# Kernel optimization log

Measured on AMD Instinct MI355X. Metric: run time of the kernel, lower is better.

Reference implementation:

```python
import jax, jax.numpy as jnp
import numpy as np
from functools import partial

BETA_F = 1.0        # layer default beta_f
DOUBLING_ITERS = 21 # covers tree depth up to 2**21; random recursive tree depth ~ O(log N)


def setup_inputs() -> dict:
    key = jax.random.key(0)
    ks = jax.random.split(key, 6)
    N, K = 2_000_000, 8
    H, W = 2048, 2048
    attrs2d = jax.random.uniform(ks[0], (N, K), dtype=jnp.float32)  # normalized attrs in [a,1]
    weight = jax.random.normal(ks[1], (K,), dtype=jnp.float32)
    bias = jax.random.normal(ks[2], (1,), dtype=jnp.float32)
    levels = jax.random.uniform(ks[3], (N,), dtype=jnp.float32)
    # valid component tree: parent[i] < i for i>0, root = 0
    u = jax.random.uniform(ks[4], (N,))
    parent = jnp.floor(u * jnp.arange(N, dtype=jnp.float32)).astype(jnp.int32)
    pixel_node = jax.random.randint(ks[5], (H, W), 0, N, dtype=jnp.int32)
    return {"attrs2d": attrs2d, "weight": weight, "bias": bias,
            "levels": levels, "parent": parent, "pixel_node": pixel_node}


def _tree_filter(sigmoid, levels, parent, pixel_node):
    """Connected (direct-rule) filtering on a component tree.

    Each node contributes sigma(node) * (level(node) - level(parent));
    the filtered value of a pixel is the sum of contributions along the
    root-to-node path (root contributes its full level).
    Path sums are computed with pointer doubling (fully vectorized).
    """
    N = levels.shape[0]
    contrib = sigmoid * (levels - levels[parent])          # (N,)
    contrib = contrib.at[0].set(levels[0])                 # root keeps its level
    # sentinel node N with zero contribution, parent of root -> sentinel
    contrib_e = jnp.concatenate([contrib, jnp.zeros((1,), contrib.dtype)])
    par_e = jnp.concatenate([parent.at[0].set(N), jnp.array([N], jnp.int32)])

    def step(carry, _):
        s, p = carry
        return (s + s[p], p[p]), None

    (s, _), _ = jax.lax.scan(step, (contrib_e, par_e), None, length=DOUBLING_ITERS)
    y_nodes = s[:N]                                        # filtered gray value per node
    return y_nodes[pixel_node]                             # (H, W)


def reference(attrs2d, weight, bias, levels, parent, pixel_node):
    logits = attrs2d @ weight + bias[0]                    # (N,)
    s = BETA_F * logits                                    # clamp_logits=False (layer default)
    sigmoid = jax.nn.sigmoid(s)
    return _tree_filter(sigmoid, levels, parent, pixel_node)
```

## Files before the change

kernel.cpp:

```cpp
#include <hip/hip_runtime.h>
#include <hip/hip_fp16.h>

typedef float vf4 __attribute__((ext_vector_type(4)));
typedef int   vi4 __attribute__((ext_vector_type(4)));

struct SP { float s; int p; };

__device__ __forceinline__ SP ldSP(const SP* __restrict__ ptr) {
    float2 v = *reinterpret_cast<const float2*>(ptr);
    SP r; r.s = v.x; r.p = __float_as_int(v.y);
    return r;
}
__device__ __forceinline__ void stSP(SP* __restrict__ ptr, float s, int p) {
    float2 v; v.x = s; v.y = __int_as_float(p);
    *reinterpret_cast<float2*>(ptr) = v;
}

__global__ void k_lev16(const float* __restrict__ levels,
                        __half* __restrict__ lev, int N) {
    int stride = gridDim.x * blockDim.x;
    int n4 = N >> 2;
    const vf4* l4 = reinterpret_cast<const vf4*>(levels);
    __half2* h2 = reinterpret_cast<__half2*>(lev);
    for (int i = blockIdx.x * blockDim.x + threadIdx.x; i < n4; i += stride) {
        vf4 v = __builtin_nontemporal_load(&l4[i]);
        __half2 h0; h0.x = __float2half(v.x); h0.y = __float2half(v.y);
        __half2 h1; h1.x = __float2half(v.z); h1.y = __float2half(v.w);
        h2[2 * i]     = h0;
        h2[2 * i + 1] = h1;
    }
    for (int i = (n4 << 2) + blockIdx.x * blockDim.x + threadIdx.x; i < N; i += stride)
        lev[i] = __float2half(levels[i]);
}

__global__ void k_contrib(const float* __restrict__ attrs,
                          const float* __restrict__ weight,
                          const float* __restrict__ bias,
                          const float* __restrict__ levels,
                          const __half* __restrict__ lev,
                          const int*   __restrict__ parent,
                          SP* __restrict__ buf, int N) {
    float w0 = weight[0], w1 = weight[1], w2 = weight[2], w3 = weight[3];
    float w4 = weight[4], w5 = weight[5], w6 = weight[6], w7 = weight[7];
    float b = bias[0];
    int stride = gridDim.x * blockDim.x;
    const vf4* a4 = reinterpret_cast<const vf4*>(attrs);
    for (int i = blockIdx.x * blockDim.x + threadIdx.x; i < N; i += stride) {
        vf4 a0 = __builtin_nontemporal_load(&a4[2 * (size_t)i]);
        vf4 a1 = __builtin_nontemporal_load(&a4[2 * (size_t)i + 1]);
        float x = a0.x * w0 + a0.y * w1 + a0.z * w2 + a0.w * w3
                + a1.x * w4 + a1.y * w5 + a1.z * w6 + a1.w * w7 + b;
        float sg = 1.0f / (1.0f + __expf(-x));
        int p = __builtin_nontemporal_load(&parent[i]);
        float c = sg * (__half2float(lev[i]) - __half2float(lev[p]));
        if (i == 0) stSP(&buf[0], levels[0], N);
        else        stSP(&buf[i], c, p);
    }
}

__global__ void k_level(const SP* __restrict__ buf,
                        __half* __restrict__ y16,
                        int lo, int hi, int N) {
    int i = lo + blockIdx.x * blockDim.x + threadIdx.x;
    if (i >= hi) return;
    float acc = 0.0f;
    int p = i;
    while (p >= lo && p < N) {
        SP w = ldSP(&buf[p]);
        acc += w.s;
        p = w.p;
    }
    if (p < lo) acc += __half2float(y16[p]);
    y16[i] = __float2half(acc);
}

__global__ void k_gather(const __half* __restrict__ y,
                         const int*   __restrict__ pix,
                         float*       __restrict__ out, int M) {
    int stride = gridDim.x * blockDim.x;
    int M8 = M >> 3;
    const vi4* pix4 = reinterpret_cast<const vi4*>(pix);
    vf4* out4 = reinterpret_cast<vf4*>(out);
    for (int g = blockIdx.x * blockDim.x + threadIdx.x; g < M8; g += stride) {
        vi4 p0 = __builtin_nontemporal_load(&pix4[2 * g]);
        vi4 p1 = __builtin_nontemporal_load(&pix4[2 * g + 1]);
        vf4 o0, o1;
        o0.x = __half2float(y[p0.x]);
        o0.y = __half2float(y[p0.y]);
        o0.z = __half2float(y[p0.z]);
        o0.w = __half2float(y[p0.w]);
        o1.x = __half2float(y[p1.x]);
        o1.y = __half2float(y[p1.y]);
        o1.z = __half2float(y[p1.z]);
        o1.w = __half2float(y[p1.w]);
        __builtin_nontemporal_store(o0, &out4[2 * g]);
        __builtin_nontemporal_store(o1, &out4[2 * g + 1]);
    }
    int tid = blockIdx.x * blockDim.x + threadIdx.x;
    for (int i = (M8 << 3) + tid; i < M; i += stride)
        out[i] = __half2float(y[pix[i]]);
}

extern "C" void kernel_launch(void* const* d_in, const int* in_sizes, int n_in,
                              void* d_out, int out_size, void* d_ws, size_t ws_size,
                              hipStream_t stream) {
    const float* attrs  = (const float*)d_in[0];
    const float* weight = (const float*)d_in[1];
    const float* bias   = (const float*)d_in[2];
    const float* levels = (const float*)d_in[3];
    const int*   parent = (const int*)d_in[4];
    const int*   pix    = (const int*)d_in[5];
    float* out = (float*)d_out;

    const int N = in_sizes[3];
    const int M = out_size;

    SP*     buf   = (SP*)d_ws;
    __half* y16   = (__half*)(buf + N);
    __half* lev16 = (__half*)(y16 + N);

    const int BLK = 256;
    #define CDIV(a,b) (((a)+(b)-1)/(b))

    k_lev16  <<<1024, BLK, 0, stream>>>(levels, lev16, N);
    k_contrib<<<2048, BLK, 0, stream>>>(attrs, weight, bias, levels, lev16, parent, buf, N);

    const int T1 = 2048, T2 = 32768, T3 = 131072, T4 = 524288, T5 = 1048576;
    k_level<<<CDIV(T1,      BLK), BLK, 0, stream>>>(buf, y16, 0,  T1, N);
    k_level<<<CDIV(T2 - T1, BLK), BLK, 0, stream>>>(buf, y16, T1, T2, N);
    k_level<<<CDIV(T3 - T2, BLK), BLK, 0, stream>>>(buf, y16, T2, T3, N);
    k_level<<<CDIV(T4 - T3, BLK), BLK, 0, stream>>>(buf, y16, T3, T4, N);
    k_level<<<CDIV(T5 - T4, BLK), BLK, 0, stream>>>(buf, y16, T4, T5, N);
    k_level<<<CDIV(N  - T5, BLK), BLK, 0, stream>>>(buf, y16, T5, N,  N);

    k_gather<<<2048, BLK, 0, stream>>>(y16, pix, out, M);
}
```

Measured before the change: 99.58 us.

## Split pixel gather into two node-range passes and merge level launches

The single pixel gather becomes two passes. The first pass gathers only nodes below the threshold into a packed fp16 scratch buffer. The second pass gathers the remaining nodes and merges them with the scratch values. The goal is to shrink the working set of each random gather so it stays in cache. The cost is reading the pixel index map twice and writing then reading the scratch buffer, and the workspace must now hold that buffer. The level-by-level path-sum launches also drop from six segments to four, which means fewer launches but longer pointer walks per thread.

```diff
diff --git a/kernel.cpp b/kernel.cpp
--- a/kernel.cpp
+++ b/kernel.cpp
@@ -74,9 +74,39 @@
     y16[i] = __float2half(acc);
 }
 
-__global__ void k_gather(const __half* __restrict__ y,
+__global__ void k_gpassA(const __half* __restrict__ y,
                          const int*   __restrict__ pix,
-                         float*       __restrict__ out, int M) {
+                         __half*      __restrict__ scratch,
+                         int M, int seg) {
+    int stride = gridDim.x * blockDim.x;
+    int M8 = M >> 3;
+    const vi4* pix4 = reinterpret_cast<const vi4*>(pix);
+    for (int g = blockIdx.x * blockDim.x + threadIdx.x; g < M8; g += stride) {
+        vi4 p0 = __builtin_nontemporal_load(&pix4[2 * g]);
+        vi4 p1 = __builtin_nontemporal_load(&pix4[2 * g + 1]);
+        __half h[8];
+        h[0] = (p0.x < seg) ? y[p0.x] : __half(0);
+        h[1] = (p0.y < seg) ? y[p0.y] : __half(0);
+        h[2] = (p0.z < seg) ? y[p0.z] : __half(0);
+        h[3] = (p0.w < seg) ? y[p0.w] : __half(0);
+        h[4] = (p1.x < seg) ? y[p1.x] : __half(0);
+        h[5] = (p1.y < seg) ? y[p1.y] : __half(0);
+        h[6] = (p1.z < seg) ? y[p1.z] : __half(0);
+        h[7] = (p1.w < seg) ? y[p1.w] : __half(0);
+        vi4 packed;
+        packed.x = (int)(((unsigned)__half_as_ushort(h[1]) << 16) | __half_as_ushort(h[0]));
+        packed.y = (int)(((unsigned)__half_as_ushort(h[3]) << 16) | __half_as_ushort(h[2]));
+        packed.z = (int)(((unsigned)__half_as_ushort(h[5]) << 16) | __half_as_ushort(h[4]));
+        packed.w = (int)(((unsigned)__half_as_ushort(h[7]) << 16) | __half_as_ushort(h[6]));
+        __builtin_nontemporal_store(packed, reinterpret_cast<vi4*>(scratch + 8 * (size_t)g));
+    }
+}
+
+__global__ void k_gpassB(const __half* __restrict__ y,
+                         const int*   __restrict__ pix,
+                         const __half* __restrict__ scratch,
+                         float*       __restrict__ out,
+                         int M, int seg) {
     int stride = gridDim.x * blockDim.x;
     int M8 = M >> 3;
     const vi4* pix4 = reinterpret_cast<const vi4*>(pix);
@@ -84,15 +114,25 @@
     for (int g = blockIdx.x * blockDim.x + threadIdx.x; g < M8; g += stride) {
         vi4 p0 = __builtin_nontemporal_load(&pix4[2 * g]);
         vi4 p1 = __builtin_nontemporal_load(&pix4[2 * g + 1]);
+        vi4 c = __builtin_nontemporal_load(reinterpret_cast<const vi4*>(scratch + 8 * (size_t)g));
+        __half ch[8];
+        ch[0] = __ushort_as_half((unsigned short)( c.x        & 0xFFFF));
+        ch[1] = __ushort_as_half((unsigned short)(((unsigned)c.x) >> 16));
+        ch[2] = __ushort_as_half((unsigned short)( c.y        & 0xFFFF));
+        ch[3] = __ushort_as_half((unsigned short)(((unsigned)c.y) >> 16));
+        ch[4] = __ushort_as_half((unsigned short)( c.z        & 0xFFFF));
+        ch[5] = __ushort_as_half((unsigned short)(((unsigned)c.z) >> 16));
+        ch[6] = __ushort_as_half((unsigned short)( c.w        & 0xFFFF));
+        ch[7] = __ushort_as_half((unsigned short)(((unsigned)c.w) >> 16));
         vf4 o0, o1;
-        o0.x = __half2float(y[p0.x]);
-        o0.y = __half2float(y[p0.y]);
-        o0.z = __half2float(y[p0.z]);
-        o0.w = __half2float(y[p0.w]);
-        o1.x = __half2float(y[p1.x]);
-        o1.y = __half2float(y[p1.y]);
-        o1.z = __half2float(y[p1.z]);
-        o1.w = __half2float(y[p1.w]);
+        o0.x = __half2float((p0.x >= seg) ? y[p0.x] : ch[0]);
+        o0.y = __half2float((p0.y >= seg) ? y[p0.y] : ch[1]);
+        o0.z = __half2float((p0.z >= seg) ? y[p0.z] : ch[2]);
+        o0.w = __half2float((p0.w >= seg) ? y[p0.w] : ch[3]);
+        o1.x = __half2float((p1.x >= seg) ? y[p1.x] : ch[4]);
+        o1.y = __half2float((p1.y >= seg) ? y[p1.y] : ch[5]);
+        o1.z = __half2float((p1.z >= seg) ? y[p1.z] : ch[6]);
+        o1.w = __half2float((p1.w >= seg) ? y[p1.w] : ch[7]);
         __builtin_nontemporal_store(o0, &out4[2 * g]);
         __builtin_nontemporal_store(o1, &out4[2 * g + 1]);
     }
@@ -115,9 +155,10 @@
     const int N = in_sizes[3];
     const int M = out_size;
 
-    SP*     buf   = (SP*)d_ws;
-    __half* y16   = (__half*)(buf + N);
-    __half* lev16 = (__half*)(y16 + N);
+    SP*     buf     = (SP*)d_ws;
+    __half* y16     = (__half*)(buf + N);
+    __half* lev16   = (__half*)(y16 + N);
+    __half* scratch = (__half*)(lev16 + N);
 
     const int BLK = 256;
     #define CDIV(a,b) (((a)+(b)-1)/(b))
@@ -125,13 +166,12 @@
     k_lev16  <<<1024, BLK, 0, stream>>>(levels, lev16, N);
     k_contrib<<<2048, BLK, 0, stream>>>(attrs, weight, bias, levels, lev16, parent, buf, N);
 
-    const int T1 = 2048, T2 = 32768, T3 = 131072, T4 = 524288, T5 = 1048576;
+    const int T1 = 32768, T2 = 524288, T3 = 1048576;
     k_level<<<CDIV(T1,      BLK), BLK, 0, stream>>>(buf, y16, 0,  T1, N);
     k_level<<<CDIV(T2 - T1, BLK), BLK, 0, stream>>>(buf, y16, T1, T2, N);
     k_level<<<CDIV(T3 - T2, BLK), BLK, 0, stream>>>(buf, y16, T2, T3, N);
-    k_level<<<CDIV(T4 - T3, BLK), BLK, 0, stream>>>(buf, y16, T3, T4, N);
-    k_level<<<CDIV(T5 - T4, BLK), BLK, 0, stream>>>(buf, y16, T4, T5, N);
-    k_level<<<CDIV(N  - T5, BLK), BLK, 0, stream>>>(buf, y16, T5, N,  N);
+    k_level<<<CDIV(N  - T3, BLK), BLK, 0, stream>>>(buf, y16, T3, N,  N);
 
-    k_gather<<<2048, BLK, 0, stream>>>(y16, pix, out, M);
+    k_gpassA<<<2048, BLK, 0, stream>>>(y16, pix, scratch, M, T3);
+    k_gpassB<<<2048, BLK, 0, stream>>>(y16, pix, scratch, out, M, T3);
 }
```

New measurement: 102.6 us. +3.0%, slower.
